# Kernel optimization log

Hardware: AMD Instinct MI355X
Metric: run time of the kernel (lower is better)

The kernel has to match this reference:

```python
import jax, jax.numpy as jnp
import numpy as np

B, T, C = 2, 2048, 2048
H, Hk, D = 32, 4, 64
N_REP = H // Hk
THETA = 10000.0


def _rope_tables():
    inv_freq = 1.0 / (THETA ** (np.arange(0, D, 2, dtype=np.float64) / D))  # [D/2]
    t = np.arange(T, dtype=np.float64)
    freqs = np.outer(t, inv_freq)                # [T, D/2]
    emb = np.repeat(freqs, 2, axis=-1)           # interleaved [T, D]
    return jnp.asarray(np.cos(emb), jnp.float32), jnp.asarray(np.sin(emb), jnp.float32)


def setup_inputs() -> dict:
    key = jax.random.key(0)
    kx, kq, kk, kv, ko = jax.random.split(key, 5)
    scale = 0.02
    x = jax.random.normal(kx, (B, T, C), jnp.float32)
    wq = jax.random.normal(kq, (H * D, C), jnp.float32) * scale
    wk = jax.random.normal(kk, (Hk * D, C), jnp.float32) * scale
    wv = jax.random.normal(kv, (Hk * D, C), jnp.float32) * scale
    wo = jax.random.normal(ko, (C, H * D), jnp.float32) * scale
    cos, sin = _rope_tables()
    return {"x": x, "cos": cos, "sin": sin, "wq": wq, "wk": wk, "wv": wv, "wo": wo}


def _apply_rope(x, cos, sin):
    # x: [B, h, T, D]; cos/sin: [T, D] interleaved
    x1 = x[..., 0::2]
    x2 = x[..., 1::2]
    rot = jnp.stack([-x2, x1], axis=-1).reshape(x.shape)
    return x * cos[None, None] + rot * sin[None, None]


def reference(x, cos, sin, wq, wk, wv, wo):
    q = (x @ wq.T).reshape(B, T, H, D).transpose(0, 2, 1, 3)    # [B,H,T,D]
    k = (x @ wk.T).reshape(B, T, Hk, D).transpose(0, 2, 1, 3)   # [B,Hk,T,D]
    v = (x @ wv.T).reshape(B, T, Hk, D).transpose(0, 2, 1, 3)   # [B,Hk,T,D]
    q = _apply_rope(q, cos, sin)
    k = _apply_rope(k, cos, sin)
    # new_cache = (k, v) pre-repeat
    kr = jnp.repeat(k, N_REP, axis=1)                            # [B,H,T,D]
    vr = jnp.repeat(v, N_REP, axis=1)
    scores = jnp.einsum('bhtd,bhsd->bhts', q, kr) / jnp.sqrt(jnp.float32(D))
    mask = jnp.tril(jnp.ones((T, T), dtype=bool))                # causal (kv_cache is None)
    scores = jnp.where(mask, scores, jnp.finfo(scores.dtype).min)
    attn = jax.nn.softmax(scores, axis=-1)
    o = jnp.einsum('bhts,bhsd->bhtd', attn, vr)
    o = o.transpose(0, 2, 1, 3).reshape(B, T, H * D)
    return (o @ wo.T, k, v)
```

## Files before the change

kernel.cpp:

```cpp
#include <hip/hip_runtime.h>
#include <hip/hip_bf16.h>

#define B_ 2
#define T_ 2048
#define C_ 2048
#define H_ 32
#define HK_ 4
#define D_ 64

typedef __attribute__((ext_vector_type(4)))  float f32x4;
typedef __attribute__((ext_vector_type(2)))  float f32x2;
typedef __attribute__((ext_vector_type(16))) float f32x16;
typedef __attribute__((ext_vector_type(8)))  short bf16x8;

static __device__ __forceinline__ unsigned short f2bf(float f) {
  union { __hip_bfloat16 h; unsigned short s; } u;
  u.h = __float2bfloat16(f);
  return u.s;
}
static __device__ __forceinline__ float bf2f(unsigned short s) {
  union { unsigned int u; float f; } u; u.u = ((unsigned int)s) << 16; return u.f;
}
static __device__ __forceinline__ unsigned int cvtpk(float lo, float hi) {
  unsigned int r;
  asm("v_cvt_pk_bf16_f32 %0, %1, %2" : "=v"(r) : "v"(lo), "v"(hi));
  return r;
}

#define GLD16(gp, lp) __builtin_amdgcn_global_load_lds( \
    (const __attribute__((address_space(1))) unsigned int*)(gp), \
    (__attribute__((address_space(3))) unsigned int*)(unsigned int)(uintptr_t)(lp), 16, 0, 0)

__global__ void f32_to_bf16(const float* __restrict__ src, unsigned short* __restrict__ dst, int n4) {
  const int i = blockIdx.x * blockDim.x + threadIdx.x;
  if (i >= n4) return;
  f32x4 v = *(const f32x4*)(src + 4 * (size_t)i);
  ushort4 o;
  o.x = f2bf(v[0]); o.y = f2bf(v[1]); o.z = f2bf(v[2]); o.w = f2bf(v[3]);
  *(ushort4*)(dst + 4 * (size_t)i) = o;
}

template<bool BF16OUT>
__global__ __launch_bounds__(256)
void gemm_bf16(const unsigned short* __restrict__ A, const unsigned short* __restrict__ W,
               void* __restrict__ Cout, int M, int N, int K) {
  __shared__ unsigned short As[128 * 32];
  __shared__ unsigned short Ws[128 * 32];

  const int tid  = threadIdx.x;
  const int lane = tid & 63;
  const int w    = tid >> 6;
  const int wm   = w >> 1, wn = w & 1;
  const int g    = lane >> 4;
  const int lr   = lane & 15;

  const int bm = blockIdx.y * 128;
  const int bn = blockIdx.x * 128;

  const int srow = lane >> 2;
  const int scol = (lane & 3) * 8;
  const unsigned short* Ag = A + (size_t)(bm + 16 * w + srow) * K + scol;
  const unsigned short* Wg = W + (size_t)(bn + 16 * w + srow) * K + scol;
  unsigned short* Asl0 = &As[(16 * w) * 32];
  unsigned short* Asl1 = &As[(64 + 16 * w) * 32];
  unsigned short* Wsl0 = &Ws[(16 * w) * 32];
  unsigned short* Wsl1 = &Ws[(64 + 16 * w) * 32];

  f32x4 acc[4][4] = {};

  for (int k0 = 0; k0 < K; k0 += 32) {
    __syncthreads();
    GLD16(Ag + k0,                    Asl0);
    GLD16(Ag + (size_t)64 * K + k0,   Asl1);
    GLD16(Wg + k0,                    Wsl0);
    GLD16(Wg + (size_t)64 * K + k0,   Wsl1);
    __syncthreads();

    bf16x8 af[4], wf[4];
#pragma unroll
    for (int m = 0; m < 4; m++)
      af[m] = *(const bf16x8*)&As[(wm * 64 + m * 16 + lr) * 32 + g * 8];
#pragma unroll
    for (int n = 0; n < 4; n++)
      wf[n] = *(const bf16x8*)&Ws[(wn * 64 + n * 16 + lr) * 32 + g * 8];
#pragma unroll
    for (int m = 0; m < 4; m++)
#pragma unroll
      for (int n = 0; n < 4; n++)
        acc[m][n] = __builtin_amdgcn_mfma_f32_16x16x32_bf16(af[m], wf[n], acc[m][n], 0, 0, 0);
  }

#pragma unroll
  for (int m = 0; m < 4; m++) {
    const int row = bm + wm * 64 + m * 16 + g * 4;
#pragma unroll
    for (int n = 0; n < 4; n++) {
      const int col = bn + wn * 64 + n * 16 + lr;
#pragma unroll
      for (int r = 0; r < 4; r++) {
        if (BF16OUT)
          ((unsigned short*)Cout)[(size_t)(row + r) * N + col] = f2bf(acc[m][n][r]);
        else
          ((float*)Cout)[(size_t)(row + r) * N + col] = acc[m][n][r];
      }
    }
  }
}

__global__ void gqa_rope_q(const unsigned short* __restrict__ qkv,
                           const float* __restrict__ cosT,
                           const float* __restrict__ sinT,
                           unsigned short* __restrict__ qb) {
  const int idx = blockIdx.x * blockDim.x + threadIdx.x;
  const int i  = idx & 31;
  const int h  = (idx >> 5) & 31;
  const int bt = idx >> 10;
  const int t  = bt & (T_ - 1);
  const int b  = bt >> 11;

  const unsigned int qv = *(const unsigned int*)(qkv + (size_t)bt * 2560 + h * D_ + 2 * i);
  const float x1 = bf2f((unsigned short)(qv & 0xffff));
  const float x2 = bf2f((unsigned short)(qv >> 16));
  const float c = cosT[t * D_ + 2 * i];
  const float s = sinT[t * D_ + 2 * i];
  const float o0 = x1 * c - x2 * s;
  const float o1 = x2 * c + x1 * s;
  const size_t o = ((size_t)(b * H_ + h) * T_ + t) * D_ + 2 * i;
  *(unsigned int*)(qb + o) = (unsigned int)f2bf(o0) | ((unsigned int)f2bf(o1) << 16);
}

__global__ void gqa_rope_k(const unsigned short* __restrict__ qkv,
                           const float* __restrict__ cosT,
                           const float* __restrict__ sinT,
                           float* __restrict__ kout,
                           unsigned short* __restrict__ kb) {
  const int idx = blockIdx.x * blockDim.x + threadIdx.x;
  const int i  = idx & 31;
  const int hk = (idx >> 5) & 3;
  const int bt = idx >> 7;
  const int t  = bt & (T_ - 1);
  const int b  = bt >> 11;

  const unsigned int kv = *(const unsigned int*)(qkv + (size_t)bt * 2560 + 2048 + hk * D_ + 2 * i);
  const float x1 = bf2f((unsigned short)(kv & 0xffff));
  const float x2 = bf2f((unsigned short)(kv >> 16));
  const float c = cosT[t * D_ + 2 * i];
  const float s = sinT[t * D_ + 2 * i];
  const float o0 = x1 * c - x2 * s;
  const float o1 = x2 * c + x1 * s;
  const size_t o = ((size_t)(b * HK_ + hk) * T_ + t) * D_ + 2 * i;
  f32x2 ov; ov[0] = o0; ov[1] = o1;
  *(f32x2*)(kout + o) = ov;
  *(unsigned int*)(kb + o) = (unsigned int)f2bf(o0) | ((unsigned int)f2bf(o1) << 16);
}

__global__ void gqa_v_reorder(const unsigned short* __restrict__ qkv,
                              float* __restrict__ vout,
                              unsigned short* __restrict__ vt) {
  const int idx = blockIdx.x * blockDim.x + threadIdx.x;
  const int d  = idx & 63;
  const int hk = (idx >> 6) & 3;
  const int bt = idx >> 8;
  const int t  = bt & (T_ - 1);
  const int b  = bt >> 11;

  const unsigned short v = qkv[(size_t)bt * 2560 + 2304 + hk * D_ + d];
  vout[((size_t)(b * HK_ + hk) * T_ + t) * D_ + d] = bf2f(v);

  const int tm   = t & 15;
  const int tpos = (t & ~15) | ((tm & 3) + ((tm >> 3) << 2) + ((tm & 4) << 1));
  vt[((size_t)(b * HK_ + hk) * D_ + d) * T_ + tpos] = v;
}

__global__ __launch_bounds__(512, 4)
void gqa_attn4(const unsigned short* __restrict__ qb,
               const unsigned short* __restrict__ kb,
               const unsigned short* __restrict__ vt,
               unsigned short* __restrict__ ob) {
  __shared__ unsigned short Ks[3][4096];
  __shared__ unsigned short Vs[3][4096];

  const int tid  = threadIdx.x;
  const int lane = tid & 63;
  const int w    = tid >> 6;
  const int qi   = lane & 31;
  const int hi   = lane >> 5;

  const int qt = 63 - (int)(blockIdx.x >> 3);
  const int go = blockIdx.x & 7;
  const int b  = go >> 2;
  const int hk = go & 3;
  const int h  = hk * 8 + w;
  const int bh = b * H_ + h;

  const int qbase = qt * 32;
  const int qrow  = qbase + qi;

  const unsigned short* qptr = qb + ((size_t)bh * T_ + qrow) * D_ + 8 * hi;
  bf16x8 qf[4];
#pragma unroll
  for (int c = 0; c < 4; c++) qf[c] = *(const bf16x8*)(qptr + 16 * c);

  const int srow   = lane >> 3;
  const int schunk = (lane & 7) ^ srow;
  const int krow   = 8 * w + srow;
  const unsigned short* gK = kb + (size_t)(b * HK_ + hk) * T_ * D_ + (size_t)krow * D_ + schunk * 8;
  const unsigned short* gV = vt + (size_t)(b * HK_ + hk) * D_ * T_ + (size_t)krow * T_ + schunk * 8;
  unsigned short* ldsK = &Ks[0][w * 512];
  unsigned short* ldsV = &Vs[0][w * 512];

#define STAGE_KV(pp, kk0) do { \
    GLD16(gK + (size_t)(kk0) * D_, ldsK + (pp) * 4096); \
    GLD16(gV + (kk0),              ldsV + (pp) * 4096); \
  } while (0)

  f32x16 o0 = {}, o1 = {};
  float m = -1e30f, l = 0.f;
  float c1 = 0.f;
  const float SC   = 0.125f * 1.44269504089f;
  const float THRR = 44.3614195f;
  const int   swz  = qi & 7;

  const int nt = ((qbase + 31) >> 6) + 1;
  STAGE_KV(0, 0);
  if (nt > 1) STAGE_KV(1, 64);

  int p = 0;
  for (int it = 0; it < nt; ++it) {
    const int kb0 = it * 64;
    const bool last = (it == nt - 1);
    const bool has1 = (kb0 + 32 <= qbase + 31);

    asm volatile("s_waitcnt lgkmcnt(0)" ::: "memory");
    if (it + 1 < nt) asm volatile("s_waitcnt vmcnt(2)" ::: "memory");
    else             asm volatile("s_waitcnt vmcnt(0)" ::: "memory");
    asm volatile("s_barrier" ::: "memory");
    if (it + 2 < nt) STAGE_KV((p + 2 > 2) ? p - 1 : p + 2, kb0 + 128);

    const unsigned short* Kt = &Ks[0][0] + p * 4096;
    const unsigned short* Vt = &Vs[0][0] + p * 4096;

    f32x16 st0 = {}, st1 = {};
    __builtin_amdgcn_s_setprio(1);
#pragma unroll
    for (int c = 0; c < 4; c++) {
      bf16x8 kf = *(const bf16x8*)&Kt[qi * 64 + (((hi + 2 * c) ^ swz) << 3)];
      st0 = __builtin_amdgcn_mfma_f32_32x32x16_bf16(kf, qf[c], st0, 0, 0, 0);
    }
    if (!last || has1) {
#pragma unroll
      for (int c = 0; c < 4; c++) {
        bf16x8 kf = *(const bf16x8*)&Kt[(32 + qi) * 64 + (((hi + 2 * c) ^ swz) << 3)];
        st1 = __builtin_amdgcn_mfma_f32_32x32x16_bf16(kf, qf[c], st1, 0, 0, 0);
      }
    }
    __builtin_amdgcn_s_setprio(0);

    if (last) {
#pragma unroll
      for (int r = 0; r < 16; ++r) {
        const int key = kb0 + (r & 3) + 8 * (r >> 2) + 4 * hi;
        st0[r] = (key      <= qrow) ? st0[r] : -1e30f;
        st1[r] = (key + 32 <= qrow) ? st1[r] : -1e30f;
      }
    }

    float tmax = fmaxf(st0[0], st0[1]);
#pragma unroll
    for (int r = 2; r < 16; ++r) tmax = fmaxf(tmax, st0[r]);
#pragma unroll
    for (int r = 0; r < 16; ++r) tmax = fmaxf(tmax, st1[r]);
    tmax = fmaxf(tmax, __shfl_xor(tmax, 32));

    if (!__all(tmax <= m + THRR)) {
      const float mnew  = fmaxf(m, tmax);
      const float al    = __builtin_amdgcn_exp2f((m - mnew) * SC);
#pragma unroll
      for (int r = 0; r < 16; ++r) { o0[r] *= al; o1[r] *= al; }
      l *= al;
      m  = mnew;
      c1 = -m * SC;
    }

    float sum = 0.f;
#pragma unroll
    for (int r = 0; r < 16; ++r) { float pv = __builtin_amdgcn_exp2f(__builtin_fmaf(st0[r], SC, c1)); st0[r] = pv; sum += pv; }
#pragma unroll
    for (int r = 0; r < 16; ++r) { float pv = __builtin_amdgcn_exp2f(__builtin_fmaf(st1[r], SC, c1)); st1[r] = pv; sum += pv; }
    sum += __shfl_xor(sum, 32);
    l += sum;

    union U8 { bf16x8 v; unsigned int u[4]; };
    U8 pf[4];
#pragma unroll
    for (int j = 0; j < 4; ++j) {
      pf[0].u[j] = cvtpk(st0[2 * j],     st0[2 * j + 1]);
      pf[1].u[j] = cvtpk(st0[8 + 2 * j], st0[8 + 2 * j + 1]);
      pf[2].u[j] = cvtpk(st1[2 * j],     st1[2 * j + 1]);
      pf[3].u[j] = cvtpk(st1[8 + 2 * j], st1[8 + 2 * j + 1]);
    }

    const int ncf = (!last || has1) ? 4 : 2;
    __builtin_amdgcn_s_setprio(1);
#pragma unroll
    for (int dh = 0; dh < 2; ++dh) {
      const unsigned short* Vrow = &Vt[(dh * 32 + qi) * 64];
      f32x16 oc = dh ? o1 : o0;
#pragma unroll
      for (int c = 0; c < 4; ++c) {
        if (c >= ncf) break;
        bf16x8 vf = *(const bf16x8*)&Vrow[(((2 * c + hi) ^ swz) << 3)];
        oc = __builtin_amdgcn_mfma_f32_32x32x16_bf16(vf, pf[c].v, oc, 0, 0, 0);
      }
      if (dh) o1 = oc; else o0 = oc;
    }
    __builtin_amdgcn_s_setprio(0);

    p = (p > 1) ? 0 : p + 1;
  }

  const float inv = 1.0f / l;
  unsigned short* orow = ob + (size_t)(b * T_ + qrow) * (H_ * D_) + h * D_;
#pragma unroll
  for (int dh = 0; dh < 2; ++dh) {
    const f32x16 ov = dh ? o1 : o0;
#pragma unroll
    for (int rg = 0; rg < 4; ++rg) {
      const int d0 = 32 * dh + 8 * rg + 4 * hi;
      ushort4 pk;
      pk.x = f2bf(ov[4 * rg + 0] * inv);
      pk.y = f2bf(ov[4 * rg + 1] * inv);
      pk.z = f2bf(ov[4 * rg + 2] * inv);
      pk.w = f2bf(ov[4 * rg + 3] * inv);
      *(ushort4*)(orow + d0) = pk;
    }
  }
#undef STAGE_KV
}

extern "C" void kernel_launch(void* const* d_in, const int* in_sizes, int n_in,
                              void* d_out, int out_size, void* d_ws, size_t ws_size,
                              hipStream_t stream) {
  const float* x    = (const float*)d_in[0];
  const float* cosT = (const float*)d_in[1];
  const float* sinT = (const float*)d_in[2];
  const float* wq   = (const float*)d_in[3];
  const float* wk   = (const float*)d_in[4];
  const float* wv   = (const float*)d_in[5];
  const float* wo   = (const float*)d_in[6];

  float* y    = (float*)d_out;
  float* kout = (float*)d_out + (size_t)B_ * T_ * C_;
  float* vout = kout + (size_t)B_ * HK_ * T_ * D_;

  char* ws = (char*)d_ws;
  unsigned short* x_bf   = (unsigned short*)(ws);
  unsigned short* q_bf   = x_bf;
  unsigned short* wqkv   = (unsigned short*)(ws + 16777216);
  unsigned short* k_bf   = wqkv;
  unsigned short* v_t    = (unsigned short*)(ws + 18874368);
  unsigned short* qkv_bf = (unsigned short*)(ws + 27262976);
  unsigned short* o_bf   = qkv_bf;
  unsigned short* wo_bf  = (unsigned short*)(ws + 48234496);

  const int M = B_ * T_;

  f32_to_bf16<<<8192, 256, 0, stream>>>(x,  x_bf, 2097152);
  f32_to_bf16<<<4096, 256, 0, stream>>>(wq, wqkv,                 1048576);
  f32_to_bf16<<<512,  256, 0, stream>>>(wk, wqkv + 2048 * 2048,   131072);
  f32_to_bf16<<<512,  256, 0, stream>>>(wv, wqkv + 2304 * 2048,   131072);

  gemm_bf16<true><<<dim3(2560 / 128, M / 128), 256, 0, stream>>>(x_bf, wqkv, qkv_bf, M, 2560, C_);

  gqa_rope_q<<<16384, 256, 0, stream>>>(qkv_bf, cosT, sinT, q_bf);
  gqa_rope_k<<<2048,  256, 0, stream>>>(qkv_bf, cosT, sinT, kout, k_bf);
  gqa_v_reorder<<<4096, 256, 0, stream>>>(qkv_bf, vout, v_t);

  f32_to_bf16<<<4096, 256, 0, stream>>>(wo, wo_bf, 1048576);

  gqa_attn4<<<512, 512, 0, stream>>>(q_bf, k_bf, v_t, o_bf);

  gemm_bf16<false><<<dim3(C_ / 128, M / 128), 256, 0, stream>>>(o_bf, wo_bf, y, M, C_, H_ * D_);
}
```

Baseline: 226.8 us.

## Triple-buffer GEMM LDS loads with swizzled layout and MFMA priority

Replaces the single-buffered bf16 GEMM with a three-stage LDS ring. Tiles are prefetched two iterations ahead via global_load_lds, with manual vmcnt waits and a single barrier per step. LDS columns are XOR-swizzled by row to cut bank conflicts on fragment reads, and s_setprio raises wave priority around the MFMA block. This hides global load latency behind compute, at the cost of triple the LDS footprint and fragile hand-tuned waitcnt counts.

```diff
diff --git a/kernel.cpp b/kernel.cpp
--- a/kernel.cpp
+++ b/kernel.cpp
@@ -41,11 +41,11 @@
 }
 
 template<bool BF16OUT>
-__global__ __launch_bounds__(256)
-void gemm_bf16(const unsigned short* __restrict__ A, const unsigned short* __restrict__ W,
-               void* __restrict__ Cout, int M, int N, int K) {
-  __shared__ unsigned short As[128 * 32];
-  __shared__ unsigned short Ws[128 * 32];
+__global__ __launch_bounds__(256, 3)
+void gemm3(const unsigned short* __restrict__ A, const unsigned short* __restrict__ W,
+           void* __restrict__ Cout, int M, int N, int K) {
+  __shared__ unsigned short As[3][128 * 32];
+  __shared__ unsigned short Ws[3][128 * 32];
 
   const int tid  = threadIdx.x;
   const int lane = tid & 63;
@@ -57,38 +57,57 @@
   const int bm = blockIdx.y * 128;
   const int bn = blockIdx.x * 128;
 
-  const int srow = lane >> 2;
-  const int scol = (lane & 3) * 8;
-  const unsigned short* Ag = A + (size_t)(bm + 16 * w + srow) * K + scol;
-  const unsigned short* Wg = W + (size_t)(bn + 16 * w + srow) * K + scol;
-  unsigned short* Asl0 = &As[(16 * w) * 32];
-  unsigned short* Asl1 = &As[(64 + 16 * w) * 32];
-  unsigned short* Wsl0 = &Ws[(16 * w) * 32];
-  unsigned short* Wsl1 = &Ws[(64 + 16 * w) * 32];
+  const int srow = tid >> 2;
+  const int sc   = (tid & 3) ^ (srow & 3);
+  const unsigned short* Ag = A + (size_t)(bm + srow) * K + sc * 8;
+  const unsigned short* Wg = W + (size_t)(bn + srow) * K + sc * 8;
+
+#define STAGE3(buf, k0) do { \
+    GLD16(Ag + (k0),                  &As[buf][       w * 512]); \
+    GLD16(Ag + (size_t)64 * K + (k0), &As[buf][2048 + w * 512]); \
+    GLD16(Wg + (k0),                  &Ws[buf][       w * 512]); \
+    GLD16(Wg + (size_t)64 * K + (k0), &Ws[buf][2048 + w * 512]); \
+  } while (0)
 
   f32x4 acc[4][4] = {};
 
-  for (int k0 = 0; k0 < K; k0 += 32) {
-    __syncthreads();
-    GLD16(Ag + k0,                    Asl0);
-    GLD16(Ag + (size_t)64 * K + k0,   Asl1);
-    GLD16(Wg + k0,                    Wsl0);
-    GLD16(Wg + (size_t)64 * K + k0,   Wsl1);
-    __syncthreads();
+  const int nt = K >> 5;
+  STAGE3(0, 0);
+  STAGE3(1, 32);
+
+  for (int t = 0; t < nt; ++t) {
+    if (t + 1 < nt) asm volatile("s_waitcnt vmcnt(4)" ::: "memory");
+    else            asm volatile("s_waitcnt vmcnt(0)" ::: "memory");
+    asm volatile("s_barrier" ::: "memory");
+
+    if (t + 2 < nt) {
+      const int nb = (t + 2) % 3;
+      STAGE3(nb, (size_t)(t + 2) * 32);
+    }
+
+    const unsigned short* At = &As[t % 3][0];
+    const unsigned short* Wt = &Ws[t % 3][0];
 
     bf16x8 af[4], wf[4];
 #pragma unroll
-    for (int m = 0; m < 4; m++)
-      af[m] = *(const bf16x8*)&As[(wm * 64 + m * 16 + lr) * 32 + g * 8];
-#pragma unroll
-    for (int n = 0; n < 4; n++)
-      wf[n] = *(const bf16x8*)&Ws[(wn * 64 + n * 16 + lr) * 32 + g * 8];
+    for (int m = 0; m < 4; m++) {
+      const int row = wm * 64 + m * 16 + lr;
+      af[m] = *(const bf16x8*)&At[row * 32 + ((g ^ (row & 3)) << 3)];
+    }
+#pragma unroll
+    for (int n = 0; n < 4; n++) {
+      const int row = wn * 64 + n * 16 + lr;
+      wf[n] = *(const bf16x8*)&Wt[row * 32 + ((g ^ (row & 3)) << 3)];
+    }
+    __builtin_amdgcn_s_setprio(1);
 #pragma unroll
     for (int m = 0; m < 4; m++)
 #pragma unroll
       for (int n = 0; n < 4; n++)
         acc[m][n] = __builtin_amdgcn_mfma_f32_16x16x32_bf16(af[m], wf[n], acc[m][n], 0, 0, 0);
+    __builtin_amdgcn_s_setprio(0);
   }
+#undef STAGE3
 
 #pragma unroll
   for (int m = 0; m < 4; m++) {
@@ -370,7 +389,7 @@
   f32_to_bf16<<<512,  256, 0, stream>>>(wk, wqkv + 2048 * 2048,   131072);
   f32_to_bf16<<<512,  256, 0, stream>>>(wv, wqkv + 2304 * 2048,   131072);
 
-  gemm_bf16<true><<<dim3(2560 / 128, M / 128), 256, 0, stream>>>(x_bf, wqkv, qkv_bf, M, 2560, C_);
+  gemm3<true><<<dim3(2560 / 128, M / 128), 256, 0, stream>>>(x_bf, wqkv, qkv_bf, M, 2560, C_);
 
   gqa_rope_q<<<16384, 256, 0, stream>>>(qkv_bf, cosT, sinT, q_bf);
   gqa_rope_k<<<2048,  256, 0, stream>>>(qkv_bf, cosT, sinT, kout, k_bf);
@@ -380,5 +399,5 @@
 
   gqa_attn4<<<512, 512, 0, stream>>>(q_bf, k_bf, v_t, o_bf);
 
-  gemm_bf16<false><<<dim3(C_ / 128, M / 128), 256, 0, stream>>>(o_bf, wo_bf, y, M, C_, H_ * D_);
-}
+  gemm3<false><<<dim3(C_ / 128, M / 128), 256, 0, stream>>>(o_bf, wo_bf, y, M, C_, H_ * D_);
+}
```

New measurement: 209.2 us. -7.8%, faster.
